# Kernel optimization log

Measured on AMD Instinct MI355X. Metric: run time of the kernel, lower is better.

The kernel has to match this reference:

```python
import jax, jax.numpy as jnp
import numpy as np

B, S, K, H, W = 64, 100, 4, 32, 32

def setup_inputs() -> dict:
    key = jax.random.key(0)
    k1, k2 = jax.random.split(key)
    output = jax.random.normal(k1, (B, S, K, H, W), dtype=jnp.float32)
    convdata = jax.random.normal(k2, (B, S, K, H, W), dtype=jnp.float32)
    return {"output": output, "convdata": convdata}

def reference(output, convdata):
    # Original: sum over 32x32 of mean(|convdata[:,:,3,i,j] - output[:,:,3,i,j]|) / 1024
    # Each (i,j) slice has identical size, so this equals a single mean of the
    # abs-diff over the whole [B, S, 32, 32] slice at channel 3.
    return jnp.mean(jnp.abs(convdata[:, :, 3] - output[:, :, 3]))
```

## Files before the change

kernel.cpp:

```cpp
#include <hip/hip_runtime.h>


#define RBLOCKS 2048
#define RTHREADS 256

__global__ __launch_bounds__(RTHREADS)
void absdiff_reduce_kernel(const float4* __restrict__ outp,
                           const float4* __restrict__ conv,
                           float* __restrict__ out,
                           int n4, float inv_total) {
    float acc0 = 0.0f, acc1 = 0.0f;
    const int stride  = gridDim.x * blockDim.x;
    const int stride2 = stride * 2;
    int v = blockIdx.x * blockDim.x + threadIdx.x;

    for (; v + stride < n4; v += stride2) {
        {
            const int pair = v >> 8;
            const size_t g = (size_t)pair * 1024 + 768 + (size_t)(v & 255);
            const float4 a = outp[g];
            const float4 b = conv[g];
            acc0 += fabsf(b.x - a.x) + fabsf(b.y - a.y)
                  + fabsf(b.z - a.z) + fabsf(b.w - a.w);
        }
        {
            const int v1 = v + stride;
            const int pair = v1 >> 8;
            const size_t g = (size_t)pair * 1024 + 768 + (size_t)(v1 & 255);
            const float4 a = outp[g];
            const float4 b = conv[g];
            acc1 += fabsf(b.x - a.x) + fabsf(b.y - a.y)
                  + fabsf(b.z - a.z) + fabsf(b.w - a.w);
        }
    }
    if (v < n4) {
        const int pair = v >> 8;
        const size_t g = (size_t)pair * 1024 + 768 + (size_t)(v & 255);
        const float4 a = outp[g];
        const float4 b = conv[g];
        acc0 += fabsf(b.x - a.x) + fabsf(b.y - a.y)
              + fabsf(b.z - a.z) + fabsf(b.w - a.w);
    }
    float acc = acc0 + acc1;

    #pragma unroll
    for (int off = 32; off > 0; off >>= 1)
        acc += __shfl_down(acc, off, 64);

    __shared__ float smem[RTHREADS / 64];
    const int lane = threadIdx.x & 63;
    const int wave = threadIdx.x >> 6;
    if (lane == 0) smem[wave] = acc;
    __syncthreads();
    if (threadIdx.x == 0) {
        float s = 0.0f;
        #pragma unroll
        for (int w = 0; w < RTHREADS / 64; ++w) s += smem[w];
        atomicAdd(out, s * inv_total);
    }
}

extern "C" void kernel_launch(void* const* d_in, const int* in_sizes, int n_in,
                              void* d_out, int out_size, void* d_ws, size_t ws_size,
                              hipStream_t stream) {
    const float4* outp = (const float4*)d_in[0];
    const float4* conv = (const float4*)d_in[1];
    float* out = (float*)d_out;

    const int n_elems = 64 * 100 * 1024;
    const int n4 = n_elems / 4;
    const float inv_total = 1.0f / (float)n_elems;

    hipMemsetAsync(out, 0, sizeof(float), stream);
    absdiff_reduce_kernel<<<RBLOCKS, RTHREADS, 0, stream>>>(outp, conv, out,
                                                            n4, inv_total);
}
```

Measured before the change: 199.7 us.

## Replace atomic accumulation with two-pass partial-sum reduction and chunk-per-block indexing

```diff
diff --git a/kernel.cpp b/kernel.cpp
--- a/kernel.cpp
+++ b/kernel.cpp
@@ -3,39 +3,30 @@
 
 #define RBLOCKS 2048
 #define RTHREADS 256
+#define NCHUNKS 6400
 
 __global__ __launch_bounds__(RTHREADS)
-void absdiff_reduce_kernel(const float4* __restrict__ outp,
-                           const float4* __restrict__ conv,
-                           float* __restrict__ out,
-                           int n4, float inv_total) {
+void absdiff_partial_kernel(const float4* __restrict__ outp,
+                            const float4* __restrict__ conv,
+                            float* __restrict__ partials) {
+    const int t = threadIdx.x;
     float acc0 = 0.0f, acc1 = 0.0f;
-    const int stride  = gridDim.x * blockDim.x;
-    const int stride2 = stride * 2;
-    int v = blockIdx.x * blockDim.x + threadIdx.x;
 
-    for (; v + stride < n4; v += stride2) {
-        {
-            const int pair = v >> 8;
-            const size_t g = (size_t)pair * 1024 + 768 + (size_t)(v & 255);
-            const float4 a = outp[g];
-            const float4 b = conv[g];
-            acc0 += fabsf(b.x - a.x) + fabsf(b.y - a.y)
-                  + fabsf(b.z - a.z) + fabsf(b.w - a.w);
-        }
-        {
-            const int v1 = v + stride;
-            const int pair = v1 >> 8;
-            const size_t g = (size_t)pair * 1024 + 768 + (size_t)(v1 & 255);
-            const float4 a = outp[g];
-            const float4 b = conv[g];
-            acc1 += fabsf(b.x - a.x) + fabsf(b.y - a.y)
-                  + fabsf(b.z - a.z) + fabsf(b.w - a.w);
-        }
+    int c = blockIdx.x;
+    for (; c + RBLOCKS < NCHUNKS; c += 2 * RBLOCKS) {
+        const size_t g0 = (size_t)c * 1024 + 768 + t;
+        const size_t g1 = (size_t)(c + RBLOCKS) * 1024 + 768 + t;
+        const float4 a0 = outp[g0];
+        const float4 b0 = conv[g0];
+        const float4 a1 = outp[g1];
+        const float4 b1 = conv[g1];
+        acc0 += fabsf(b0.x - a0.x) + fabsf(b0.y - a0.y)
+              + fabsf(b0.z - a0.z) + fabsf(b0.w - a0.w);
+        acc1 += fabsf(b1.x - a1.x) + fabsf(b1.y - a1.y)
+              + fabsf(b1.z - a1.z) + fabsf(b1.w - a1.w);
     }
-    if (v < n4) {
-        const int pair = v >> 8;
-        const size_t g = (size_t)pair * 1024 + 768 + (size_t)(v & 255);
+    if (c < NCHUNKS) {
+        const size_t g = (size_t)c * 1024 + 768 + t;
         const float4 a = outp[g];
         const float4 b = conv[g];
         acc0 += fabsf(b.x - a.x) + fabsf(b.y - a.y)
@@ -48,6 +39,29 @@
         acc += __shfl_down(acc, off, 64);
 
     __shared__ float smem[RTHREADS / 64];
+    const int lane = t & 63;
+    const int wave = t >> 6;
+    if (lane == 0) smem[wave] = acc;
+    __syncthreads();
+    if (t == 0) {
+        float s = 0.0f;
+        #pragma unroll
+        for (int w = 0; w < RTHREADS / 64; ++w) s += smem[w];
+        partials[blockIdx.x] = s;
+    }
+}
+
+__global__ __launch_bounds__(RTHREADS)
+void final_reduce_kernel(const float* __restrict__ partials,
+                         float* __restrict__ out, float inv_total) {
+    float acc = 0.0f;
+    #pragma unroll
+    for (int i = 0; i < RBLOCKS / RTHREADS; ++i)
+        acc += partials[threadIdx.x + i * RTHREADS];
+    #pragma unroll
+    for (int off = 32; off > 0; off >>= 1)
+        acc += __shfl_down(acc, off, 64);
+    __shared__ float smem[RTHREADS / 64];
     const int lane = threadIdx.x & 63;
     const int wave = threadIdx.x >> 6;
     if (lane == 0) smem[wave] = acc;
@@ -56,7 +70,7 @@
         float s = 0.0f;
         #pragma unroll
         for (int w = 0; w < RTHREADS / 64; ++w) s += smem[w];
-        atomicAdd(out, s * inv_total);
+        out[0] = s * inv_total;
     }
 }
 
@@ -65,13 +79,11 @@
                               hipStream_t stream) {
     const float4* outp = (const float4*)d_in[0];
     const float4* conv = (const float4*)d_in[1];
+    float* partials = (float*)d_ws;
     float* out = (float*)d_out;
 
-    const int n_elems = 64 * 100 * 1024;
-    const int n4 = n_elems / 4;
-    const float inv_total = 1.0f / (float)n_elems;
+    const float inv_total = 1.0f / (float)(64 * 100 * 1024);
 
-    hipMemsetAsync(out, 0, sizeof(float), stream);
-    absdiff_reduce_kernel<<<RBLOCKS, RTHREADS, 0, stream>>>(outp, conv, out,
-                                                            n4, inv_total);
+    absdiff_partial_kernel<<<RBLOCKS, RTHREADS, 0, stream>>>(outp, conv, partials);
+    final_reduce_kernel<<<1, RTHREADS, 0, stream>>>(partials, out, inv_total);
 }
```

Result: faster. 180.7 us (median of 2 runs) (-9.5%).
